# Kernel tuning notes

Hardware: AMD Instinct MI355X
Metric: run time of the kernel (lower is better)

## Reference

```python
import jax, jax.numpy as jnp
import numpy as np

LAG = 24      # lag (months of 20 days) in the train window
STEP = 20     # days per rebalancing step
ANNUAL = 252.0


def setup_inputs() -> dict:
    key = jax.random.key(0)
    Y = jax.random.normal(key, (20480, 128), dtype=jnp.float32) * 0.01  # daily returns
    a = jnp.full((1,), 0.997, dtype=jnp.float32)                        # EWMA decay param
    logridge = jnp.full((1,), float(np.log(1e-5)), dtype=jnp.float32)   # log ridge param
    return {"Y": Y, "a": a, "logridge": logridge}


def reference(Y, a, logridge):
    n, p = Y.shape
    W = n // STEP - LAG            # number of rolling windows (1000)
    T = LAG * STEP                 # train window length (480)
    a0 = a[0]
    ridge = jnp.exp(logridge[0])

    # EWMA weights: w_t = a^(T-1-t) (most recent day has weight 1), normalized to sum T
    expo = jnp.arange(T - 1, -1, -1, dtype=Y.dtype)
    w = a0 ** expo
    w = w / w.sum() * T
    wsum = w.sum()
    denom = 1.0 - (w * w).sum() / (T * T)   # bias correction (w**2 / T**2).sum()
    ones_p = jnp.ones((p,), Y.dtype)

    def per_window(j):
        # train: Y[(i-lag)*20 : i*20] with i = j + LAG  ->  rows [j*20, j*20+T)
        Yt = jax.lax.dynamic_slice(Y, (j * STEP, 0), (T, p))
        # test: Y[i*20 : (i+1)*20]
        Yte = jax.lax.dynamic_slice(Y, ((j + LAG) * STEP, 0), (STEP, p))
        mean = (w[:, None] * Yt).sum(axis=0) / wsum          # [p]
        Yc = Yt - mean[None, :]                               # [T, p]
        Sigma = (Yc.T @ (w[:, None] * Yc)) / T / denom        # [p, p] weighted covariance
        lam, U = jnp.linalg.eigh(Sigma)
        Pmat = (U / (ridge + lam)[None, :]) @ U.T             # ridge-shrunk precision
        # GMV weights: P @ 1 / (1' P 1)
        v = Pmat @ ones_p
        wgt = v / (ones_p @ v)
        ret = Yte @ wgt                                       # [STEP] portfolio returns
        e = ret.sum()                                         # cumulative test return
        s = (ret * ret).mean()                                # realized daily variance
        return e, s

    e_all, s_all = jax.vmap(per_window)(jnp.arange(W))
    vol = jnp.sqrt(s_all.mean() * ANNUAL)
    mu = e_all.mean() / STEP * ANNUAL
    sharpe = mu / vol
    return vol, mu, sharpe
```

## Files before the change

kernel.cpp:

```cpp
#include <hip/hip_runtime.h>
#include <math.h>

#define P 128
#define T_WIN 480
#define STEPD 20
#define LAG_W 24
#define NITER 14
#define SEG 64
#define PACK 8448
#define PCHUNK 33

__device__ __forceinline__ int tri_off(int r) {
  const int a = r >> 2, b = r & 3;
  return ((a + 1) * (2 * a + b)) << 2;
}

__device__ __forceinline__ void ewma_consts(float af, double& la, float& Sf, float& denomf) {
  const double a = (double)af;
  la = log(a);
  const double A480 = exp(480.0 * la);
  const double S = (1.0 - A480) / (1.0 - a);
  const double Su2 = (1.0 - A480 * A480) / (1.0 - a * a);
  Sf = (float)S;
  denomf = (float)(1.0 - Su2 / (S * S));
}

__global__ __launch_bounds__(256) void cblocks_kernel(const float* __restrict__ Y,
                                                      const float* __restrict__ aarg,
                                                      float* __restrict__ cvec,
                                                      float* __restrict__ Call, int K) {
  const int k = blockIdx.x;
  const int tid = threadIdx.x;
  const int ti = tid >> 4, tj = tid & 15;
  __shared__ float st[STEPD][P];
  __shared__ float sbwsm[STEPD];
  if (tid < STEPD) {
    const double la = log((double)aarg[0]);
    sbwsm[tid] = (float)exp(0.5 * (double)(STEPD - 1 - tid) * la);
  }
  __syncthreads();
  const float* __restrict__ Yb = Y + (size_t)k * STEPD * P;
  for (int i = tid; i < STEPD * P / 4; i += 256) {
    float4 v = ((const float4*)Yb)[i];
    const float sw = sbwsm[i >> 5];
    v.x *= sw; v.y *= sw; v.z *= sw; v.w *= sw;
    ((float4*)&st[0][0])[i] = v;
  }
  __syncthreads();

  float acc[8][8];
#pragma unroll
  for (int u = 0; u < 8; ++u)
#pragma unroll
    for (int v = 0; v < 8; ++v) acc[u][v] = 0.0f;

#pragma unroll 4
  for (int t = 0; t < STEPD; ++t) {
    float af[8], bf[8];
    *(float4*)(af)     = *(const float4*)&st[t][ti * 4];
    *(float4*)(af + 4) = *(const float4*)&st[t][64 + ti * 4];
    *(float4*)(bf)     = *(const float4*)&st[t][tj * 4];
    *(float4*)(bf + 4) = *(const float4*)&st[t][64 + tj * 4];
#pragma unroll
    for (int u = 0; u < 8; ++u)
#pragma unroll
      for (int v = 0; v < 8; ++v) acc[u][v] += af[u] * bf[v];
  }

  float* __restrict__ Ck = Call + (size_t)k * PACK;
#pragma unroll
  for (int u = 0; u < 8; ++u) {
    const int r = (u < 4) ? (ti * 4 + u) : (64 + ti * 4 + u - 4);
    const int offr = tri_off(r);
    if (tj * 4 <= r) {
      float4 o0;
      o0.x = acc[u][0]; o0.y = acc[u][1]; o0.z = acc[u][2]; o0.w = acc[u][3];
      *(float4*)(Ck + offr + tj * 4) = o0;
    }
    if (64 + tj * 4 <= r) {
      float4 o1;
      o1.x = acc[u][4]; o1.y = acc[u][5]; o1.z = acc[u][6]; o1.w = acc[u][7];
      *(float4*)(Ck + offr + 64 + tj * 4) = o1;
    }
  }
  if (tid < P) {
    float s = 0.0f;
    for (int t = 0; t < STEPD; ++t) s += sbwsm[t] * st[t][tid];
    cvec[(size_t)k * P + tid] = s;
  }
}

__global__ __launch_bounds__(256) void scan_kernel(float* __restrict__ Call,
                                                   const float* __restrict__ aarg) {
  __shared__ float asm_[SEG];
  const int tid = threadIdx.x;
  const int seg = blockIdx.x / PCHUNK;
  const int chunk = blockIdx.x - seg * PCHUNK;
  if (tid < SEG) {
    const double la = log((double)aarg[0]);
    asm_[tid] = (float)exp(-(double)(20 * tid) * la);
  }
  __syncthreads();
  const int e = chunk * 256 + tid;
  float* __restrict__ base = Call + ((size_t)seg * SEG) * PACK + e;
  float g = 0.0f;
#pragma unroll 4
  for (int k = 0; k < SEG; ++k) {
    const float c = base[(size_t)k * PACK];
    g = fmaf(asm_[k], c, g);
    base[(size_t)k * PACK] = g;
  }
}

__global__ __launch_bounds__(128, 2) void window12_kernel(
    const float* __restrict__ Y, const float* __restrict__ aarg,
    const float* __restrict__ logridge, const float* __restrict__ cvec,
    const float* __restrict__ Gall, float* __restrict__ e_all,
    float* __restrict__ s_all, int W) {
  const int bid = blockIdx.x;
  const int q = W >> 3, r8 = W & 7;
  const int xcd = bid & 7, idx = bid >> 3;
  const int j = ((xcd < r8) ? (xcd * (q + 1)) : (r8 * (q + 1) + (xcd - r8) * q)) + idx;

  const int tid = threadIdx.x;
  const int ti = tid >> 4, tj = tid & 15;
  const int lane = tid & 63;
  const int wv = tid >> 6;
  const int rowbase = ti * 16;

  __shared__ float Gsm[PACK];
  __shared__ float rsm[P];
  __shared__ float wsm[P];
  __shared__ float vsm[P];
  __shared__ float meansm[P];
  __shared__ float coefsm[LAG_W];
  __shared__ float2 gd_wave[2];
  __shared__ float rs_wave[2];
  __shared__ float retd[STEPD];

  double la_d;
  float S, denom;
  ewma_consts(aarg[0], la_d, S, denom);
  const float ridge = expf(logridge[0]);

  if (tid < LAG_W)
    coefsm[tid] = (float)exp((double)(STEPD * (LAG_W - 1 - tid)) * la_d);
  __syncthreads();

  int offR[16];
#pragma unroll
  for (int u = 0; u < 16; ++u) offR[u] = tri_off(rowbase + u);
  int colv[8], offC[8];
#pragma unroll
  for (int v = 0; v < 8; ++v) {
    colv[v] = (v < 4) ? (tj * 4 + v) : (64 + tj * 4 + (v - 4));
    offC[v] = tri_off(colv[v]);
  }

  int mats[3];
  float scls[3];
  int nm = 0;
  {
    const int o1 = j & ~(SEG - 1);
    const int end = j + 23;
    const int b = o1 + SEG;
    const float pA = (float)exp((double)(STEPD * (end - o1)) * la_d);
    if (end < b) {
      mats[nm] = end; scls[nm] = pA; ++nm;
      if (j > o1) { mats[nm] = j - 1; scls[nm] = -pA; ++nm; }
    } else {
      const float pB2 = (float)exp((double)(STEPD * (end - b)) * la_d);
      mats[nm] = b - 1; scls[nm] = pA; ++nm;
      if (j > o1) { mats[nm] = j - 1; scls[nm] = -pA; ++nm; }
      mats[nm] = end; scls[nm] = pB2; ++nm;
    }
  }

  {
    float4* __restrict__ Gsm4 = (float4*)Gsm;
    if (nm == 3) {
      const float cf0 = scls[0], cf1 = scls[1], cf2 = scls[2];
      const float4* __restrict__ G0 = (const float4*)(Gall + (size_t)mats[0] * PACK);
      const float4* __restrict__ G1 = (const float4*)(Gall + (size_t)mats[1] * PACK);
      const float4* __restrict__ G2 = (const float4*)(Gall + (size_t)mats[2] * PACK);
      for (int i = tid; i < PACK / 4; i += 128) {
        const float4 a0 = G0[i];
        const float4 a1 = G1[i];
        const float4 a2 = G2[i];
        float4 o;
        o.x = cf0 * a0.x + cf1 * a1.x + cf2 * a2.x;
        o.y = cf0 * a0.y + cf1 * a1.y + cf2 * a2.y;
        o.z = cf0 * a0.z + cf1 * a1.z + cf2 * a2.z;
        o.w = cf0 * a0.w + cf1 * a1.w + cf2 * a2.w;
        Gsm4[i] = o;
      }
    } else {
      const float cf0 = scls[0];
      const float cf1 = (nm > 1) ? scls[1] : 0.0f;
      const float4* __restrict__ G0 = (const float4*)(Gall + (size_t)mats[0] * PACK);
      const float4* __restrict__ G1 = (const float4*)(Gall + (size_t)mats[(nm > 1) ? 1 : 0] * PACK);
      for (int i = tid; i < PACK / 4; i += 128) {
        const float4 a0 = G0[i];
        const float4 a1 = G1[i];
        float4 o;
        o.x = cf0 * a0.x + cf1 * a1.x;
        o.y = cf0 * a0.y + cf1 * a1.y;
        o.z = cf0 * a0.z + cf1 * a1.z;
        o.w = cf0 * a0.w + cf1 * a1.w;
        Gsm4[i] = o;
      }
    }
  }

  {
    float s = 0.0f;
    for (int m = 0; m < LAG_W; ++m) s += coefsm[m] * cvec[(size_t)(j + m) * P + tid];
    meansm[tid] = s;
    rsm[tid] = 1.0f;
  }
  __syncthreads();

  float acc[16][8];
  {
    const float sc1 = 1.0f / (S * denom);
    const float sc2 = 1.0f / (S * S * denom);
#pragma unroll
    for (int u = 0; u < 16; ++u) {
      const int r = rowbase + u;
      const int offr = offR[u];
      const float mr = meansm[r] * sc2;
#pragma unroll
      for (int v = 0; v < 8; ++v) {
        const int c = colv[v];
        const int idxe = (c <= r) ? (offr + c) : (offC[v] + r);
        float mval = Gsm[idxe] * sc1 - mr * meansm[c];
        if (r == c) mval += ridge;
        acc[u][v] = mval;
      }
    }
  }
  __syncthreads();

  float xo = 0.0f, ro = 1.0f, po = 0.0f, so = 0.0f;
  float gam_old = 1.0f, alp_old = 1.0f;

  for (int it = 0; it < NITER; ++it) {
    const float4 p0 = *(const float4*)&rsm[tj * 4];
    const float4 p1 = *(const float4*)&rsm[64 + tj * 4];
    float pv[8] = {p0.x, p0.y, p0.z, p0.w, p1.x, p1.y, p1.z, p1.w};
    float ap[16];
#pragma unroll
    for (int u = 0; u < 16; ++u) {
      float s = 0.0f;
#pragma unroll
      for (int v = 0; v < 8; ++v) s += acc[u][v] * pv[v];
      ap[u] = s;
    }
#pragma unroll
    for (int m = 1; m <= 8; m <<= 1) {
#pragma unroll
      for (int u = 0; u < 16; ++u) ap[u] += __shfl_xor(ap[u], m);
    }
    if (tj == 0) {
#pragma unroll
      for (int u = 0; u < 16; ++u) wsm[rowbase + u] = ap[u];
    }
    {
      const float4 r0 = *(const float4*)&rsm[rowbase];
      const float4 r1 = *(const float4*)&rsm[rowbase + 4];
      const float4 r2 = *(const float4*)&rsm[rowbase + 8];
      const float4 r3 = *(const float4*)&rsm[rowbase + 12];
      const float rv[16] = {r0.x, r0.y, r0.z, r0.w, r1.x, r1.y, r1.z, r1.w,
                            r2.x, r2.y, r2.z, r2.w, r3.x, r3.y, r3.z, r3.w};
      float gp = 0.0f, dp = 0.0f;
#pragma unroll
      for (int u = 0; u < 16; ++u) {
        gp = fmaf(rv[u], rv[u], gp);
        dp = fmaf(ap[u], rv[u], dp);
      }
      gp += __shfl_down(gp, 16); dp += __shfl_down(dp, 16);
      gp += __shfl_down(gp, 32); dp += __shfl_down(dp, 32);
      if (lane == 0) { gd_wave[wv].x = gp; gd_wave[wv].y = dp; }
    }
    __syncthreads();

    const float gam = gd_wave[0].x + gd_wave[1].x;
    const float del = gd_wave[0].y + gd_wave[1].y;
    float bet, alp;
    if (it == 0) { bet = 0.0f; alp = gam / del; }
    else {
      bet = gam / gam_old;
      alp = gam / (del - bet * gam / alp_old);
    }
    gam_old = gam; alp_old = alp;

    const float wv_c = wsm[tid];
    po = ro + bet * po;
    so = wv_c + bet * so;
    xo += alp * po;
    ro -= alp * so;
    rsm[tid] = ro;
    __syncthreads();
  }

  vsm[tid] = xo;
  float sv = xo;
#pragma unroll
  for (int m = 32; m > 0; m >>= 1) sv += __shfl_down(sv, m);
  if (lane == 0) rs_wave[wv] = sv;
  __syncthreads();
  const float sumv = rs_wave[0] + rs_wave[1];

  const float* __restrict__ Yte = Y + (size_t)(j + LAG_W) * STEPD * P;
  for (int d = wv; d < STEPD; d += 2) {
    float pp = Yte[(size_t)d * P + lane] * vsm[lane] +
               Yte[(size_t)d * P + 64 + lane] * vsm[64 + lane];
    for (int off = 32; off > 0; off >>= 1) pp += __shfl_down(pp, off);
    if (lane == 0) retd[d] = pp;
  }
  __syncthreads();

  if (tid == 0) {
    const float invs = 1.0f / sumv;
    float e = 0.0f, s = 0.0f;
#pragma unroll
    for (int d = 0; d < STEPD; ++d) {
      const float rr = retd[d] * invs;
      e += rr; s += rr * rr;
    }
    e_all[j] = e;
    s_all[j] = s * (1.0f / (float)STEPD);
  }
}

__global__ __launch_bounds__(256, 2) void window_fallback(
    const float* __restrict__ Y, const float* __restrict__ aarg,
    const float* __restrict__ logridge, float* __restrict__ e_all,
    float* __restrict__ s_all, int W) {
  const int j = blockIdx.x;
  const int tid = threadIdx.x;
  const int ti = tid >> 4;
  const int tj = tid & 15;

  __shared__ float Msm[P][P + 1];
  __shared__ float wsm[T_WIN];
  __shared__ float swsm[T_WIN];
  __shared__ float meansm[P];
  __shared__ float red[256];
  __shared__ float retd[STEPD];
  __shared__ float zsm[P];
  __shared__ float vsm[P];
  __shared__ float bsm[P];

  float* stage = &Msm[0][0];

  double la;
  float S, denom;
  ewma_consts(aarg[0], la, S, denom);
  for (int t = tid; t < T_WIN; t += 256) {
    const double wn = exp((double)(T_WIN - 1 - t) * la) / (double)S * (double)T_WIN;
    wsm[t] = (float)wn;
    swsm[t] = (float)sqrt(wn);
  }
  if (tid < P) bsm[tid] = 1.0f;
  const float ridge = expf(logridge[0]);
  __syncthreads();

  const float* __restrict__ Ywin = Y + (size_t)j * STEPD * P;
  {
    const int col = tid & 127;
    const int half = tid >> 7;
    float m = 0.0f;
    const int t0 = half * (T_WIN / 2), t1 = t0 + T_WIN / 2;
    for (int t = t0; t < t1; ++t) m += wsm[t] * Ywin[(size_t)t * P + col];
    red[tid] = m;
    __syncthreads();
    if (tid < P) meansm[tid] = (red[tid] + red[tid + 128]) * (1.0f / (float)T_WIN);
    __syncthreads();
  }

  float acc[8][8];
#pragma unroll
  for (int u = 0; u < 8; ++u)
#pragma unroll
    for (int v = 0; v < 8; ++v) acc[u][v] = 0.0f;

  for (int c = 0; c < T_WIN / 32; ++c) {
    __syncthreads();
#pragma unroll
    for (int i = 0; i < 4; ++i) {
      const int idx = i * 1024 + tid * 4;
      float4 v = *(const float4*)(Ywin + (size_t)c * 32 * P + idx);
      const float sw = swsm[c * 32 + (idx >> 7)];
      v.x *= sw; v.y *= sw; v.z *= sw; v.w *= sw;
      *(float4*)(stage + idx) = v;
    }
    __syncthreads();
#pragma unroll 4
    for (int t = 0; t < 32; ++t) {
      const float* rowp = stage + t * P;
      float af[8], bf[8];
      *(float4*)(af) = *(const float4*)(rowp + ti * 8);
      *(float4*)(af + 4) = *(const float4*)(rowp + ti * 8 + 4);
      *(float4*)(bf) = *(const float4*)(rowp + tj * 8);
      *(float4*)(bf + 4) = *(const float4*)(rowp + tj * 8 + 4);
#pragma unroll
      for (int u = 0; u < 8; ++u)
#pragma unroll
        for (int v = 0; v < 8; ++v) acc[u][v] += af[u] * bf[v];
    }
  }
  __syncthreads();

  const float invTd = 1.0f / ((float)T_WIN * denom);
#pragma unroll
  for (int u = 0; u < 8; ++u) {
    const int r = ti * 8 + u;
    const float mr = meansm[r];
#pragma unroll
    for (int v = 0; v < 8; ++v) {
      const int cc = tj * 8 + v;
      float m = (acc[u][v] - (float)T_WIN * mr * meansm[cc]) * invTd;
      if (r == cc) m += ridge;
      Msm[r][cc] = m;
    }
  }
  __syncthreads();

  for (int k = 0; k < P; ++k) {
    const float dkk = Msm[k][k];
    const float sq = sqrtf(dkk);
    const float invd = 1.0f / sq;
    if (tid == 0) Msm[k][k] = sq;
    const int i = k + 1 + tid;
    if (i < P) Msm[i][k] *= invd;
    __syncthreads();
    const int nrem = P - 1 - k;
    for (int ii = ti; ii < nrem; ii += 16) {
      const int ri = k + 1 + ii;
      const float Lik = Msm[ri][k];
      for (int jj = tj; jj < nrem; jj += 16) {
        const int cj = k + 1 + jj;
        Msm[ri][cj] -= Lik * Msm[cj][k];
      }
    }
    __syncthreads();
  }

  for (int k = 0; k < P; ++k) {
    const float zk = bsm[k] / Msm[k][k];
    if (tid == 0) zsm[k] = zk;
    const int i = k + 1 + tid;
    if (i < P) bsm[i] -= Msm[i][k] * zk;
    __syncthreads();
  }
  for (int k = P - 1; k >= 0; --k) {
    const float vk = zsm[k] / Msm[k][k];
    if (tid == 0) vsm[k] = vk;
    if (tid < k) zsm[tid] -= Msm[k][tid] * vk;
    __syncthreads();
  }

  red[tid] = (tid < P) ? vsm[tid] : 0.0f;
  __syncthreads();
  for (int off = 128; off > 0; off >>= 1) {
    if (tid < off) red[tid] += red[tid + off];
    __syncthreads();
  }

  const float* __restrict__ Yte = Y + (size_t)(j + LAG_W) * STEPD * P;
  const int wv = tid >> 6;
  const int lane = tid & 63;
  for (int d = wv; d < STEPD; d += 4) {
    float pp = Yte[(size_t)d * P + lane] * vsm[lane] +
               Yte[(size_t)d * P + 64 + lane] * vsm[64 + lane];
    for (int off = 32; off > 0; off >>= 1) pp += __shfl_down(pp, off);
    if (lane == 0) retd[d] = pp;
  }
  __syncthreads();

  if (tid == 0) {
    const float invs = 1.0f / red[0];
    float e = 0.0f, s = 0.0f;
#pragma unroll
    for (int d = 0; d < STEPD; ++d) {
      const float r = retd[d] * invs;
      e += r;
      s += r * r;
    }
    e_all[j] = e;
    s_all[j] = s * (1.0f / (float)STEPD);
  }
}

__global__ __launch_bounds__(256) void final_kernel(const float* __restrict__ e_all,
                                                    const float* __restrict__ s_all,
                                                    float* __restrict__ out, int W) {
  __shared__ float r1[256], r2[256];
  const int tid = threadIdx.x;
  float e = 0.0f, s = 0.0f;
  for (int i = tid; i < W; i += 256) {
    e += e_all[i];
    s += s_all[i];
  }
  r1[tid] = e;
  r2[tid] = s;
  __syncthreads();
  for (int off = 128; off > 0; off >>= 1) {
    if (tid < off) {
      r1[tid] += r1[tid + off];
      r2[tid] += r2[tid + off];
    }
    __syncthreads();
  }
  if (tid == 0) {
    const float vol = sqrtf(r2[0] / (float)W * 252.0f);
    const float mu = r1[0] / (float)W / (float)STEPD * 252.0f;
    out[0] = vol;
    out[1] = mu;
    out[2] = mu / vol;
  }
}

extern "C" void kernel_launch(void* const* d_in, const int* in_sizes, int n_in,
                              void* d_out, int out_size, void* d_ws, size_t ws_size,
                              hipStream_t stream) {
  const float* Y = (const float*)d_in[0];
  const float* a = (const float*)d_in[1];
  const float* logridge = (const float*)d_in[2];
  float* out = (float*)d_out;

  const int n = in_sizes[0] / P;
  const int K = n / STEPD;
  const int W = K - LAG_W;

  float* ws = (float*)d_ws;
  float* e_all = ws;
  float* s_all = ws + 1024;
  float* cvec = ws + 2048;
  float* Gall = ws + 2048 + (size_t)K * P;

  const size_t need = ((size_t)2048 + (size_t)K * P + (size_t)K * PACK) * sizeof(float);

  if (ws_size >= need && (n % STEPD) == 0 && W > 0 && W <= 1024 && (K % SEG) == 0) {
    cblocks_kernel<<<K, 256, 0, stream>>>(Y, a, cvec, Gall, K);
    scan_kernel<<<(K / SEG) * PCHUNK, 256, 0, stream>>>(Gall, a);
    window12_kernel<<<W, 128, 0, stream>>>(Y, a, logridge, cvec, Gall, e_all, s_all, W);
  } else {
    window_fallback<<<W, 256, 0, stream>>>(Y, a, logridge, e_all, s_all, W);
  }
  final_kernel<<<1, 256, 0, stream>>>(e_all, s_all, out, W);
}
```

Baseline: 84.33 us.

## Fuse final reduction via atomics, drop wsm shared staging, cut CG iterations

Cuts the conjugate-gradient iteration count from 14 to 12, which loosens the solve tolerance and reduces per-window work. It replaces the shared-memory staging of the matrix-vector product with a register select over the shuffled partial sums. It also removes the separate final kernel by accumulating e and s with atomics and letting the last block compute the outputs, at the cost of an added memset. Fewer iterations risks accuracy, and atomic float summation makes the result order-dependent.

Result: slower. 113.1 us (+34.1%).

```diff
diff --git a/kernel.cpp b/kernel.cpp
--- a/kernel.cpp
+++ b/kernel.cpp
@@ -5,7 +5,7 @@
 #define T_WIN 480
 #define STEPD 20
 #define LAG_W 24
-#define NITER 14
+#define NITER 12
 #define SEG 64
 #define PACK 8448
 #define PCHUNK 33
@@ -112,11 +112,11 @@
   }
 }
 
-__global__ __launch_bounds__(128, 2) void window12_kernel(
+__global__ __launch_bounds__(128, 2) void window13_kernel(
     const float* __restrict__ Y, const float* __restrict__ aarg,
     const float* __restrict__ logridge, const float* __restrict__ cvec,
-    const float* __restrict__ Gall, float* __restrict__ e_all,
-    float* __restrict__ s_all, int W) {
+    const float* __restrict__ Gall, float* __restrict__ accum,
+    float* __restrict__ out, int W) {
   const int bid = blockIdx.x;
   const int q = W >> 3, r8 = W & 7;
   const int xcd = bid & 7, idx = bid >> 3;
@@ -130,7 +130,6 @@
 
   __shared__ float Gsm[PACK];
   __shared__ float rsm[P];
-  __shared__ float wsm[P];
   __shared__ float vsm[P];
   __shared__ float meansm[P];
   __shared__ float coefsm[LAG_W];
@@ -261,10 +260,10 @@
 #pragma unroll
       for (int u = 0; u < 16; ++u) ap[u] += __shfl_xor(ap[u], m);
     }
-    if (tj == 0) {
-#pragma unroll
-      for (int u = 0; u < 16; ++u) wsm[rowbase + u] = ap[u];
-    }
+    float wv_c = ap[0];
+#pragma unroll
+    for (int u = 1; u < 16; ++u) wv_c = (tj == u) ? ap[u] : wv_c;
+
     {
       const float4 r0 = *(const float4*)&rsm[rowbase];
       const float4 r1 = *(const float4*)&rsm[rowbase + 4];
@@ -294,7 +293,6 @@
     }
     gam_old = gam; alp_old = alp;
 
-    const float wv_c = wsm[tid];
     po = ro + bet * po;
     so = wv_c + bet * so;
     xo += alp * po;
@@ -328,8 +326,19 @@
       const float rr = retd[d] * invs;
       e += rr; s += rr * rr;
     }
-    e_all[j] = e;
-    s_all[j] = s * (1.0f / (float)STEPD);
+    atomicAdd(&accum[0], e);
+    atomicAdd(&accum[1], s * (1.0f / (float)STEPD));
+    __threadfence();
+    const int old = atomicAdd((int*)&accum[2], 1);
+    if (old == W - 1) {
+      const float es = atomicAdd(&accum[0], 0.0f);
+      const float ss = atomicAdd(&accum[1], 0.0f);
+      const float vol = sqrtf(ss / (float)W * 252.0f);
+      const float mu = es / (float)W / (float)STEPD * 252.0f;
+      out[0] = vol;
+      out[1] = mu;
+      out[2] = mu / vol;
+    }
   }
 }
 
@@ -535,19 +544,21 @@
   const int W = K - LAG_W;
 
   float* ws = (float*)d_ws;
-  float* e_all = ws;
-  float* s_all = ws + 1024;
-  float* cvec = ws + 2048;
-  float* Gall = ws + 2048 + (size_t)K * P;
-
-  const size_t need = ((size_t)2048 + (size_t)K * P + (size_t)K * PACK) * sizeof(float);
+  float* accum = ws;
+  float* e_all = ws + 1024;
+  float* s_all = ws + 2048;
+  float* cvec = ws + 4096;
+  float* Gall = ws + 4096 + (size_t)K * P;
+
+  const size_t need = ((size_t)4096 + (size_t)K * P + (size_t)K * PACK) * sizeof(float);
 
   if (ws_size >= need && (n % STEPD) == 0 && W > 0 && W <= 1024 && (K % SEG) == 0) {
+    hipMemsetAsync(accum, 0, 4 * sizeof(float), stream);
     cblocks_kernel<<<K, 256, 0, stream>>>(Y, a, cvec, Gall, K);
     scan_kernel<<<(K / SEG) * PCHUNK, 256, 0, stream>>>(Gall, a);
-    window12_kernel<<<W, 128, 0, stream>>>(Y, a, logridge, cvec, Gall, e_all, s_all, W);
+    window13_kernel<<<W, 128, 0, stream>>>(Y, a, logridge, cvec, Gall, accum, out, W);
   } else {
     window_fallback<<<W, 256, 0, stream>>>(Y, a, logridge, e_all, s_all, W);
-  }
-  final_kernel<<<1, 256, 0, stream>>>(e_all, s_all, out, W);
-}
+    final_kernel<<<1, 256, 0, stream>>>(e_all, s_all, out, W);
+  }
+}
```
